# Kernel optimization log

Hardware: AMD Instinct MI355X
Metric: run time of the kernel (lower is better)

Reference implementation:

```python
import jax, jax.numpy as jnp
import numpy as np

NUM_KEYS = 100000
NUM_VALUES = 100000
KEY_SIZE = 256
VALUE_SIZE = 256
B = 4096
K = 50


def setup_inputs() -> dict:
    key = jax.random.key(0)
    k1, k2, k3, k4, k5, k6 = jax.random.split(key, 6)
    keys = jax.random.randint(k1, (B, K), 0, NUM_KEYS, dtype=jnp.int64 if jax.config.jax_enable_x64 else jnp.int32)
    values = jax.random.randint(k2, (B, K), 0, NUM_VALUES, dtype=keys.dtype)
    pair_length = jnp.maximum(jax.random.randint(k3, (B,), 0, K, dtype=keys.dtype), 1)
    query = jax.random.normal(k4, (B, KEY_SIZE), dtype=jnp.float32)
    key_table = jax.random.normal(k5, (NUM_KEYS, KEY_SIZE), dtype=jnp.float32)
    value_table = jax.random.normal(k6, (NUM_VALUES, VALUE_SIZE), dtype=jnp.float32)
    return {"keys": keys, "values": values, "pair_length": pair_length,
            "query": query, "key_table": key_table, "value_table": value_table}


def reference(keys, values, pair_length, query, key_table, value_table):
    # Gather per-example key/value embeddings: (B, K, D)
    k_emb = key_table[keys]
    v_emb = value_table[values]
    # Scores: query . key_emb -> (B, K)
    logits = jnp.einsum('bd,bkd->bk', query, k_emb)
    # Mask positions >= pair_length, then stable softmax over valid entries
    mask = jnp.arange(k_emb.shape[1])[None, :] < pair_length[:, None]
    neg_inf = jnp.finfo(logits.dtype).min
    prob = jax.nn.softmax(jnp.where(mask, logits, neg_inf), axis=1)
    # Weighted value sum -> (B, value_size)
    knowledge = jnp.einsum('bk,bkd->bd', prob, v_emb)
    return knowledge
```

## Files before the change

kernel.cpp:

```cpp
#include <hip/hip_runtime.h>
#include <math.h>

#define BATCH 4096
#define KMAX 50
#define DIM 256
#define NITER 13

__global__ __launch_bounds__(256) void kv_memory_kernel(
    const int* __restrict__ keys,
    const int* __restrict__ values,
    const int* __restrict__ pair_len,
    const float* __restrict__ query,
    const float* __restrict__ key_table,
    const float* __restrict__ value_table,
    float* __restrict__ out)
{
    const int b    = blockIdx.x;
    const int tid  = threadIdx.x;
    const int lane = tid & 63;
    const int wave = tid >> 6;

    __shared__ int    s_keys[KMAX];
    __shared__ int    s_vals[KMAX];
    __shared__ float  s_logit[64];
    __shared__ float4 s_acc[4][64];

    int len = pair_len[b];
    if (len < 1) len = 1;
    if (len > KMAX) len = KMAX;

    if (tid < KMAX) {
        s_keys[tid] = keys[b * KMAX + tid];
        s_vals[tid] = values[b * KMAX + tid];
    }

    const float4 q = *reinterpret_cast<const float4*>(query + (size_t)b * DIM + lane * 4);
    __syncthreads();

    int kidx[NITER], vidx[NITER];
    #pragma unroll
    for (int i = 0; i < NITER; ++i) {
        const int k  = wave + 4 * i;
        const int kc = (k < len) ? k : (len - 1);
        kidx[i] = s_keys[kc];
        vidx[i] = s_vals[kc];
    }

    float4 vr[NITER];
    #pragma unroll
    for (int i = 0; i < NITER; ++i) {
        vr[i] = *reinterpret_cast<const float4*>(
            value_table + (size_t)vidx[i] * DIM + lane * 4);
    }
    float4 kr[NITER];
    #pragma unroll
    for (int i = 0; i < NITER; ++i) {
        kr[i] = *reinterpret_cast<const float4*>(
            key_table + (size_t)kidx[i] * DIM + lane * 4);
    }

    float dot[NITER];
    #pragma unroll
    for (int i = 0; i < NITER; ++i) {
        dot[i] = q.x * kr[i].x + q.y * kr[i].y + q.z * kr[i].z + q.w * kr[i].w;
    }
    #pragma unroll
    for (int off = 32; off; off >>= 1) {
        #pragma unroll
        for (int i = 0; i < NITER; ++i) dot[i] += __shfl_xor(dot[i], off);
    }
    if (lane == 0) {
        #pragma unroll
        for (int i = 0; i < NITER; ++i) {
            const int k = wave + 4 * i;
            s_logit[k] = dot[i];
        }
    }
    __syncthreads();

    float lg = (lane < len) ? s_logit[lane] : -INFINITY;
    float m = lg;
    #pragma unroll
    for (int off = 32; off; off >>= 1) m = fmaxf(m, __shfl_xor(m, off));
    float e = (lane < len) ? __expf(lg - m) : 0.0f;
    float s = e;
    #pragma unroll
    for (int off = 32; off; off >>= 1) s += __shfl_xor(s, off);
    const float p = e * (1.0f / s);

    float4 acc = make_float4(0.f, 0.f, 0.f, 0.f);
    #pragma unroll
    for (int i = 0; i < NITER; ++i) {
        const int k = wave + 4 * i;
        const float w = __shfl(p, (k < 63) ? k : 63);
        acc.x += w * vr[i].x;
        acc.y += w * vr[i].y;
        acc.z += w * vr[i].z;
        acc.w += w * vr[i].w;
    }
    s_acc[wave][lane] = acc;
    __syncthreads();

    if (wave == 0) {
        float4 a0 = s_acc[0][lane];
        const float4 a1 = s_acc[1][lane];
        const float4 a2 = s_acc[2][lane];
        const float4 a3 = s_acc[3][lane];
        a0.x += a1.x + a2.x + a3.x;
        a0.y += a1.y + a2.y + a3.y;
        a0.z += a1.z + a2.z + a3.z;
        a0.w += a1.w + a2.w + a3.w;
        *reinterpret_cast<float4*>(out + (size_t)b * DIM + lane * 4) = a0;
    }
}

extern "C" void kernel_launch(void* const* d_in, const int* in_sizes, int n_in,
                              void* d_out, int out_size, void* d_ws, size_t ws_size,
                              hipStream_t stream) {
    const int*   keys        = (const int*)d_in[0];
    const int*   values      = (const int*)d_in[1];
    const int*   pair_len    = (const int*)d_in[2];
    const float* query       = (const float*)d_in[3];
    const float* key_table   = (const float*)d_in[4];
    const float* value_table = (const float*)d_in[5];
    float* out = (float*)d_out;

    kv_memory_kernel<<<BATCH, 256, 0, stream>>>(
        keys, values, pair_len, query, key_table, value_table, out);
}
```

Measured before the change: 36.64 us.

## Map one wave per batch row and skip key/value gathers beyond pair length

Each wave now handles a whole batch row instead of four waves sharing one row. This removes shared memory, block barriers and the cross-wave reduction. Keys and value rows are gathered in chunks of 10, and chunks at or past the valid length are skipped, so masked entries are no longer fetched. In exchange each wave issues its gathers in a longer serial chain with less memory-level parallelism per row, and the two phases (keys, then values) no longer overlap their loads.

```diff
diff --git a/kernel.cpp b/kernel.cpp
--- a/kernel.cpp
+++ b/kernel.cpp
@@ -4,7 +4,7 @@
 #define BATCH 4096
 #define KMAX 50
 #define DIM 256
-#define NITER 13
+#define BK 10
 
 __global__ __launch_bounds__(256) void kv_memory_kernel(
     const int* __restrict__ keys,
@@ -15,74 +15,53 @@
     const float* __restrict__ value_table,
     float* __restrict__ out)
 {
-    const int b    = blockIdx.x;
-    const int tid  = threadIdx.x;
-    const int lane = tid & 63;
-    const int wave = tid >> 6;
-
-    __shared__ int    s_keys[KMAX];
-    __shared__ int    s_vals[KMAX];
-    __shared__ float  s_logit[64];
-    __shared__ float4 s_acc[4][64];
+    const int lane = threadIdx.x & 63;
+    const int wave = threadIdx.x >> 6;
+    const int b    = blockIdx.x * 4 + wave;
 
     int len = pair_len[b];
-    if (len < 1) len = 1;
-    if (len > KMAX) len = KMAX;
+    len = (len < 1) ? 1 : (len > KMAX ? KMAX : len);
 
-    if (tid < KMAX) {
-        s_keys[tid] = keys[b * KMAX + tid];
-        s_vals[tid] = values[b * KMAX + tid];
+    const int li = (lane < KMAX) ? lane : (KMAX - 1);
+    const int kk = keys[(size_t)b * KMAX + li];
+    const int vv = values[(size_t)b * KMAX + li];
+
+    const float4 q = *reinterpret_cast<const float4*>(query + (size_t)b * DIM + lane * 4);
+
+    float lg = -INFINITY;
+    #pragma unroll
+    for (int kb = 0; kb < KMAX; kb += BK) {
+        if (kb < len) {
+            float4 kr[BK];
+            #pragma unroll
+            for (int j = 0; j < BK; ++j) {
+                const int k  = kb + j;
+                const int kc = (k < len) ? k : (len - 1);
+                const int idx = __shfl(kk, kc);
+                kr[j] = *reinterpret_cast<const float4*>(
+                    key_table + (size_t)idx * DIM + lane * 4);
+            }
+            float d[BK];
+            #pragma unroll
+            for (int j = 0; j < BK; ++j)
+                d[j] = q.x * kr[j].x + q.y * kr[j].y + q.z * kr[j].z + q.w * kr[j].w;
+            #pragma unroll
+            for (int off = 32; off; off >>= 1) {
+                #pragma unroll
+                for (int j = 0; j < BK; ++j) d[j] += __shfl_xor(d[j], off);
+            }
+            #pragma unroll
+            for (int j = 0; j < BK; ++j) {
+                const int k = kb + j;
+                if (k < len && lane == k) lg = d[j];
+            }
+        }
     }
 
-    const float4 q = *reinterpret_cast<const float4*>(query + (size_t)b * DIM + lane * 4);
-    __syncthreads();
-
-    int kidx[NITER], vidx[NITER];
-    #pragma unroll
-    for (int i = 0; i < NITER; ++i) {
-        const int k  = wave + 4 * i;
-        const int kc = (k < len) ? k : (len - 1);
-        kidx[i] = s_keys[kc];
-        vidx[i] = s_vals[kc];
-    }
-
-    float4 vr[NITER];
-    #pragma unroll
-    for (int i = 0; i < NITER; ++i) {
-        vr[i] = *reinterpret_cast<const float4*>(
-            value_table + (size_t)vidx[i] * DIM + lane * 4);
-    }
-    float4 kr[NITER];
-    #pragma unroll
-    for (int i = 0; i < NITER; ++i) {
-        kr[i] = *reinterpret_cast<const float4*>(
-            key_table + (size_t)kidx[i] * DIM + lane * 4);
-    }
-
-    float dot[NITER];
-    #pragma unroll
-    for (int i = 0; i < NITER; ++i) {
-        dot[i] = q.x * kr[i].x + q.y * kr[i].y + q.z * kr[i].z + q.w * kr[i].w;
-    }
-    #pragma unroll
-    for (int off = 32; off; off >>= 1) {
-        #pragma unroll
-        for (int i = 0; i < NITER; ++i) dot[i] += __shfl_xor(dot[i], off);
-    }
-    if (lane == 0) {
-        #pragma unroll
-        for (int i = 0; i < NITER; ++i) {
-            const int k = wave + 4 * i;
-            s_logit[k] = dot[i];
-        }
-    }
-    __syncthreads();
-
-    float lg = (lane < len) ? s_logit[lane] : -INFINITY;
     float m = lg;
     #pragma unroll
     for (int off = 32; off; off >>= 1) m = fmaxf(m, __shfl_xor(m, off));
-    float e = (lane < len) ? __expf(lg - m) : 0.0f;
+    float e = __expf(lg - m);
     float s = e;
     #pragma unroll
     for (int off = 32; off; off >>= 1) s += __shfl_xor(s, off);
@@ -90,28 +69,30 @@
 
     float4 acc = make_float4(0.f, 0.f, 0.f, 0.f);
     #pragma unroll
-    for (int i = 0; i < NITER; ++i) {
-        const int k = wave + 4 * i;
-        const float w = __shfl(p, (k < 63) ? k : 63);
-        acc.x += w * vr[i].x;
-        acc.y += w * vr[i].y;
-        acc.z += w * vr[i].z;
-        acc.w += w * vr[i].w;
+    for (int kb = 0; kb < KMAX; kb += BK) {
+        if (kb < len) {
+            float4 vr[BK];
+            float  w[BK];
+            #pragma unroll
+            for (int j = 0; j < BK; ++j) {
+                const int k  = kb + j;
+                const int kc = (k < len) ? k : (len - 1);
+                const int idx = __shfl(vv, kc);
+                vr[j] = *reinterpret_cast<const float4*>(
+                    value_table + (size_t)idx * DIM + lane * 4);
+                w[j] = (k < len) ? __shfl(p, k) : 0.0f;
+            }
+            #pragma unroll
+            for (int j = 0; j < BK; ++j) {
+                acc.x += w[j] * vr[j].x;
+                acc.y += w[j] * vr[j].y;
+                acc.z += w[j] * vr[j].z;
+                acc.w += w[j] * vr[j].w;
+            }
+        }
     }
-    s_acc[wave][lane] = acc;
-    __syncthreads();
 
-    if (wave == 0) {
-        float4 a0 = s_acc[0][lane];
-        const float4 a1 = s_acc[1][lane];
-        const float4 a2 = s_acc[2][lane];
-        const float4 a3 = s_acc[3][lane];
-        a0.x += a1.x + a2.x + a3.x;
-        a0.y += a1.y + a2.y + a3.y;
-        a0.z += a1.z + a2.z + a3.z;
-        a0.w += a1.w + a2.w + a3.w;
-        *reinterpret_cast<float4*>(out + (size_t)b * DIM + lane * 4) = a0;
-    }
+    *reinterpret_cast<float4*>(out + (size_t)b * DIM + lane * 4) = acc;
 }
 
 extern "C" void kernel_launch(void* const* d_in, const int* in_sizes, int n_in,
@@ -125,6 +106,6 @@
     const float* value_table = (const float*)d_in[5];
     float* out = (float*)d_out;
 
-    kv_memory_kernel<<<BATCH, 256, 0, stream>>>(
+    kv_memory_kernel<<<BATCH / 4, 256, 0, stream>>>(
         keys, values, pair_len, query, key_table, value_table, out);
 }
```

Result: slower. 40.17 us (+9.6%).
